# Kernel tuning notes

Hardware: AMD Instinct MI355X
Metric: run time of the kernel (lower is better)

The kernel has to match this reference:

```python
import jax, jax.numpy as jnp
import numpy as np

BN_EPS = 1e-5
DIST_EPS = 1e-8


def setup_inputs() -> dict:
    key = jax.random.key(0)
    ks = jax.random.split(key, 10)
    B, Ni, Mi = 4, 16384, 4096
    C1, C2 = 64, 64
    Cin = C1 + C2  # 128, mlp=[128,128,128]
    inp = {
        "unknown": jax.random.normal(ks[0], (B * Ni, 3), dtype=jnp.float32),
        "unknown_batch_cnt": np.full(B, Ni, dtype=np.int64),
        "known": jax.random.normal(ks[1], (B * Mi, 3), dtype=jnp.float32),
        "known_batch_cnt": np.full(B, Mi, dtype=np.int64),
        "unknown_feats": jax.random.normal(ks[2], (B * Ni, C1), dtype=jnp.float32),
        "known_feats": jax.random.normal(ks[3], (B * Mi, C2), dtype=jnp.float32),
        "W1": jax.random.normal(ks[4], (128, Cin), dtype=jnp.float32) * 0.05,
        "g1": jnp.ones((128,), dtype=jnp.float32),
        "b1": jnp.zeros((128,), dtype=jnp.float32),
        "W2": jax.random.normal(ks[5], (128, 128), dtype=jnp.float32) * 0.05,
        "g2": jnp.ones((128,), dtype=jnp.float32),
        "b2": jnp.zeros((128,), dtype=jnp.float32),
    }
    return inp


def _three_nn(u, k):
    # u: (B,Ni,3), k: (B,Mi,3) -> dist (B,Ni,3), idx (B,Ni,3) within each batch
    d2 = (jnp.sum(u * u, -1)[:, :, None] + jnp.sum(k * k, -1)[:, None, :]
          - 2.0 * jnp.einsum("bnd,bmd->bnm", u, k))  # (B,Ni,Mi)
    neg_d2, idx = jax.lax.top_k(-d2, 3)
    dist = jnp.sqrt(jnp.maximum(-neg_d2, 0.0))
    return dist, idx


def _bn_relu(y, g, b):
    # BatchNorm2d over the point dim (training-mode batch stats), then ReLU
    mu = jnp.mean(y, axis=0)
    var = jnp.mean((y - mu) ** 2, axis=0)
    return jax.nn.relu((y - mu) * jax.lax.rsqrt(var + BN_EPS) * g + b)


def reference(unknown, unknown_batch_cnt, known, known_batch_cnt,
              unknown_feats, known_feats, W1, g1, b1, W2, g2, b2):
    ucnt = np.asarray(unknown_batch_cnt)
    kcnt = np.asarray(known_batch_cnt)
    B = ucnt.shape[0]
    Ni, Mi = int(ucnt[0]), int(kcnt[0])  # equal-count ragged batches
    C2 = known_feats.shape[1]

    u = unknown.reshape(B, Ni, 3)
    k = known.reshape(B, Mi, 3)
    dist, idx = _three_nn(u, k)

    dist_recip = 1.0 / (dist + DIST_EPS)
    weight = dist_recip / jnp.sum(dist_recip, axis=-1, keepdims=True)  # (B,Ni,3)

    kf = known_feats.reshape(B, Mi, C2)
    gathered = kf[jnp.arange(B)[:, None, None], idx]  # (B,Ni,3,C2)
    interp = jnp.sum(weight[..., None] * gathered, axis=2).reshape(B * Ni, C2)

    x = jnp.concatenate([interp, unknown_feats], axis=1)  # (N, C2+C1)
    x = _bn_relu(x @ W1.T, g1, b1)
    x = _bn_relu(x @ W2.T, g2, b2)
    return x
```

## Files before the change

### kernel.cpp

```cpp
#include <hip/hip_runtime.h>
#include <hip/hip_bf16.h>

#define GRID  32
#define NCELL (GRID * GRID * GRID)
#define H     0.3125f
#define INVH  3.2f
#define OFF   5.0f
#define SUBW  8
#define XPAD  136
#define NREP  16

using f32x4  = __attribute__((ext_vector_type(4))) float;
using bf16x8 = __attribute__((ext_vector_type(8))) short;

static __device__ inline short f2bs(float f) {
  __hip_bfloat16 h = __float2bfloat16(f);
  return __builtin_bit_cast(short, h);
}
static __device__ inline float bs2f(short s) {
  return __bfloat162float(__builtin_bit_cast(__hip_bfloat16, s));
}
static __device__ inline int cellco(float x) {
  int c = (int)((x + OFF) * INVH);
  return min(GRID - 1, max(0, c));
}

#define INSF(dv, mv)                                   \
  {                                                    \
    bool q0 = dv < b0, q1 = dv < b1, q2 = dv < b2;     \
    float P0 = b0, P1 = b1; int Q0 = j0, Q1 = j1;      \
    b2 = q1 ? P1 : (q2 ? dv : b2);                     \
    j2 = q1 ? Q1 : (q2 ? mv : j2);                     \
    b1 = q0 ? P0 : (q1 ? dv : P1);                     \
    j1 = q0 ? Q0 : (q1 ? mv : Q1);                     \
    b0 = q0 ? dv : P0;                                 \
    j0 = q0 ? mv : Q0;                                 \
  }

#define MERGE3(lo_mk, hi_mk)                                                        \
  for (int mk = lo_mk; mk <= hi_mk; mk <<= 1) {                                     \
    float ob0 = __shfl_xor(b0, mk), ob1 = __shfl_xor(b1, mk), ob2 = __shfl_xor(b2, mk); \
    int   oj0 = __shfl_xor(j0, mk), oj1 = __shfl_xor(j1, mk), oj2 = __shfl_xor(j2, mk); \
    INSF(ob0, oj0); INSF(ob1, oj1); INSF(ob2, oj2);                                 \
  }

__global__ __launch_bounds__(256) void zero_k(int4* __restrict__ dst, int n4) {
  int i = blockIdx.x * 256 + threadIdx.x;
  if (i < n4) dst[i] = int4{0, 0, 0, 0};
}

__global__ __launch_bounds__(256) void hist_k(
    const float* __restrict__ known, int Mtot, int Mi,
    const float* __restrict__ unknown, int Ntot,
    int* __restrict__ khist, int* __restrict__ qhist,
    int* __restrict__ kcell, int* __restrict__ qcell,
    const float* __restrict__ W1, const float* __restrict__ W2,
    __hip_bfloat16* __restrict__ Wb1, __hip_bfloat16* __restrict__ Wb2) {
  int i = blockIdx.x * 256 + threadIdx.x;
  if (i < 128 * 128) {
    Wb1[i] = __float2bfloat16(W1[i]);
    Wb2[i] = __float2bfloat16(W2[i]);
  }
  if (i < Mtot) {
    int b = i / Mi;
    float x = known[(size_t)i * 3], y = known[(size_t)i * 3 + 1], z = known[(size_t)i * 3 + 2];
    int c = b * NCELL + (cellco(z) * GRID + cellco(y)) * GRID + cellco(x);
    kcell[i] = c;
    atomicAdd(&khist[c], 1);
  }
  if (i < Ntot) {
    int Ni = Ntot / (Mtot / Mi);
    int b = i / Ni;
    float x = unknown[(size_t)i * 3], y = unknown[(size_t)i * 3 + 1], z = unknown[(size_t)i * 3 + 2];
    int c = b * NCELL + (cellco(z) * GRID + cellco(y)) * GRID + cellco(x);
    qcell[i] = c;
    atomicAdd(&qhist[c], 1);
  }
}

__global__ __launch_bounds__(256) void scan1_k(
    const int4* __restrict__ Hc4, int* __restrict__ bsum) {
  __shared__ int sh[256];
  int t = threadIdx.x;
  int4 h = Hc4[blockIdx.x * 256 + t];
  int s = h.x + h.y + h.z + h.w;
  sh[t] = s;
  __syncthreads();
  for (int d = 128; d > 0; d >>= 1) {
    if (t < d) sh[t] += sh[t + d];
    __syncthreads();
  }
  if (t == 0) bsum[blockIdx.x] = sh[0];
}

__global__ __launch_bounds__(256) void scan2_k(
    int* __restrict__ bsum, int nb, int* __restrict__ kstart, int* __restrict__ qstart,
    int nc, int Mtot, int Ntot) {
  __shared__ int sh[256];
  int t = threadIdx.x;
  int v = (t < nb) ? bsum[t] : 0;
  sh[t] = v;
  __syncthreads();
  for (int d = 1; d < 256; d <<= 1) {
    int u = (t >= d) ? sh[t - d] : 0;
    __syncthreads();
    sh[t] += u;
    __syncthreads();
  }
  if (t < nb) bsum[t] = sh[t] - v;
  if (t == 0) { kstart[nc] = Mtot; qstart[nc] = Ntot; }
}

__global__ __launch_bounds__(256) void scan3_k(
    const int4* __restrict__ Hc4, const int* __restrict__ bsum,
    int* __restrict__ kstart, int* __restrict__ kfill,
    int* __restrict__ qstart, int* __restrict__ qfill, int nc, int Mtot) {
  __shared__ int sh[256];
  int t = threadIdx.x;
  int g4 = blockIdx.x * 256 + t;
  int4 h = Hc4[g4];
  int s = h.x + h.y + h.z + h.w;
  sh[t] = s;
  __syncthreads();
  for (int d = 1; d < 256; d <<= 1) {
    int u = (t >= d) ? sh[t - d] : 0;
    __syncthreads();
    sh[t] += u;
    __syncthreads();
  }
  int run = bsum[blockIdx.x] + sh[t] - s;
  int hv[4] = {h.x, h.y, h.z, h.w};
#pragma unroll
  for (int j = 0; j < 4; ++j) {
    int g = g4 * 4 + j;
    if (g < nc) { kstart[g] = run; kfill[g] = run; }
    else        { int q = g - nc; qstart[q] = run - Mtot; qfill[q] = run - Mtot; }
    run += hv[j];
  }
}

__global__ __launch_bounds__(256) void scatter_k(
    const float* __restrict__ known, int Mtot, int Mi,
    const float* __restrict__ unknown, int Ntot,
    const int* __restrict__ kcell, const int* __restrict__ qcell,
    int* __restrict__ kfill, int* __restrict__ qfill,
    f32x4* __restrict__ k4s, int* __restrict__ korder,
    f32x4* __restrict__ u4s, int* __restrict__ qorder) {
  int i = blockIdx.x * 256 + threadIdx.x;
  if (i < Mtot) {
    int slot = atomicAdd(&kfill[kcell[i]], 1);
    float x = known[(size_t)i * 3], y = known[(size_t)i * 3 + 1], z = known[(size_t)i * 3 + 2];
    f32x4 v;
    v[0] = -2.f * x; v[1] = -2.f * y; v[2] = -2.f * z;
    v[3] = x * x + y * y + z * z;
    k4s[slot] = v;
    korder[slot] = i - (i / Mi) * Mi;
  }
  if (i < Ntot) {
    int slot = atomicAdd(&qfill[qcell[i]], 1);
    float x = unknown[(size_t)i * 3], y = unknown[(size_t)i * 3 + 1], z = unknown[(size_t)i * 3 + 2];
    f32x4 v;
    v[0] = x; v[1] = y; v[2] = z;
    v[3] = __fmaf_rn(x, x, __fmaf_rn(y, y, z * z));
    u4s[slot] = v;
    qorder[slot] = i;
  }
}

static __device__ __forceinline__ void scan_box_strided(
    int R, int sub, int stride, int cx, int cy, int cz, int cellbase,
    const int* __restrict__ cstart, const f32x4* __restrict__ k4s,
    const int* __restrict__ korder,
    float ux, float uy, float uz,
    float& b0, float& b1, float& b2, int& j0, int& j1, int& j2) {
  int zlo = max(cz - R, 0), zhi = min(cz + R, GRID - 1);
  int ylo = max(cy - R, 0), yhi = min(cy + R, GRID - 1);
  int xlo = max(cx - R, 0), xhi = min(cx + R, GRID - 1);
  int ny = yhi - ylo + 1;
  int nrows = (zhi - zlo + 1) * ny;
  for (int rid = sub; rid < nrows; rid += stride) {
    int zz = rid / ny;
    int y  = ylo + (rid - zz * ny);
    int row = cellbase + ((zlo + zz) * GRID + y) * GRID;
    int s = cstart[row + xlo];
    int e = cstart[row + xhi + 1];
    for (int i = s; i < e; ++i) {
      f32x4 k = k4s[i];
      float d = __fmaf_rn(ux, k[0], __fmaf_rn(uy, k[1], __fmaf_rn(uz, k[2], k[3])));
      int m = korder[i];
      INSF(d, m);
    }
  }
}

__global__ __launch_bounds__(256) void knn_grid_k(
    const f32x4* __restrict__ u4s, const int* __restrict__ qorder,
    const int* __restrict__ cstart, const f32x4* __restrict__ k4s,
    const int* __restrict__ korder, int Ni,
    float* __restrict__ w, int* __restrict__ idx,
    int* __restrict__ rcnt, int* __restrict__ rlist, float* __restrict__ rd3) {
  int nwc = gridDim.x * 4;
  int gw  = blockIdx.x * 4 + (threadIdx.x >> 6);
  int wchunk = (gw * 997) & (nwc - 1);
  int s   = wchunk * 8 + ((threadIdx.x & 63) / SUBW);
  int sub = threadIdx.x & (SUBW - 1);
  f32x4 u4 = u4s[s];
  int p = qorder[s];
  int b = p / Ni;
  float ux = u4[0], uy = u4[1], uz = u4[2], uu = u4[3];
  int cx = cellco(ux), cy = cellco(uy), cz = cellco(uz);
  int cellbase = b * NCELL;
  int xlo = max(cx - 1, 0), xhi = min(cx + 1, GRID - 1);

  int cs[9], ce[9];
#pragma unroll
  for (int q = 0; q < 9; ++q) {
    int z = cz + (q / 3) - 1;
    int y = cy + (q % 3) - 1;
    bool valid = ((unsigned)z < GRID) && ((unsigned)y < GRID);
    int row = cellbase + (z * GRID + y) * GRID;
    int a0 = valid ? row + xlo : cellbase;
    int a1 = valid ? row + xhi + 1 : cellbase;
    cs[q] = cstart[a0];
    ce[q] = cstart[a1];
  }

  float b0 = 3e38f, b1 = 3e38f, b2 = 3e38f;
  int   j0 = 0,     j1 = 0,     j2 = 0;
#pragma unroll
  for (int q = 0; q < 9; ++q) {
    for (int i = cs[q] + sub; i < ce[q]; i += SUBW) {
      f32x4 k = k4s[i];
      float d = __fmaf_rn(ux, k[0], __fmaf_rn(uy, k[1], __fmaf_rn(uz, k[2], k[3])));
      int m = korder[i];
      INSF(d, m);
    }
  }
  MERGE3(1, SUBW / 2);

  float d3sq = b2 + uu;
  bool ok = d3sq <= H * H;

  if (sub == 0) {
    if (ok) {
      float d0 = sqrtf(fmaxf(b0 + uu, 0.f));
      float d1 = sqrtf(fmaxf(b1 + uu, 0.f));
      float d2 = sqrtf(fmaxf(b2 + uu, 0.f));
      float r0 = 1.f / (d0 + 1e-8f);
      float r1 = 1.f / (d1 + 1e-8f);
      float r2 = 1.f / (d2 + 1e-8f);
      float rs = 1.f / (r0 + r1 + r2);
      size_t o = (size_t)p * 3;
      w[o] = r0 * rs; w[o + 1] = r1 * rs; w[o + 2] = r2 * rs;
      idx[o] = j0; idx[o + 1] = j1; idx[o + 2] = j2;
    } else {
      int t = atomicAdd(rcnt, 1);
      rlist[t] = s;
      rd3[t] = d3sq;
    }
  }
}

__global__ __launch_bounds__(256) void knn_retry_k(
    const f32x4* __restrict__ u4s, const int* __restrict__ qorder,
    const int* __restrict__ rlist, const float* __restrict__ rd3,
    const int* __restrict__ rcnt,
    const int* __restrict__ cstart, const f32x4* __restrict__ k4s,
    const int* __restrict__ korder, int Ni,
    float* __restrict__ w, int* __restrict__ idx) {
  int lane = threadIdx.x & 63;
  int wv   = blockIdx.x * 4 + (threadIdx.x >> 6);
  int nw   = gridDim.x * 4;
  int cnt  = rcnt[0];
  for (int q = wv; q < cnt; q += nw) {
    int sq = rlist[q];
    f32x4 u4 = u4s[sq];
    int p = qorder[sq];
    int b = p / Ni;
    float ux = u4[0], uy = u4[1], uz = u4[2], uu = u4[3];
    int cx = cellco(ux), cy = cellco(uy), cz = cellco(uz);
    int cellbase = b * NCELL;

    float d3sq = rd3[q];
    int Rc = 1;
    float b0, b1, b2; int j0, j1, j2;
    bool ok = false;
    while (!ok) {
      if (d3sq < 1e30f) {
        Rc = max((int)ceilf(sqrtf(fmaxf(d3sq, 0.f)) * INVH), Rc + 1);
      } else {
        Rc = Rc * 2;
      }
      Rc = min(Rc, GRID);
      b0 = b1 = b2 = 3e38f; j0 = j1 = j2 = 0;
      scan_box_strided(Rc, lane, 64, cx, cy, cz, cellbase, cstart, k4s, korder,
                       ux, uy, uz, b0, b1, b2, j0, j1, j2);
      MERGE3(1, 32);
      d3sq = b2 + uu;
      float cov = (float)Rc * H;
      ok = (d3sq <= cov * cov) || (Rc >= GRID);
    }
    if (lane == 0) {
      float d0 = sqrtf(fmaxf(b0 + uu, 0.f));
      float d1 = sqrtf(fmaxf(b1 + uu, 0.f));
      float d2 = sqrtf(fmaxf(b2 + uu, 0.f));
      float r0 = 1.f / (d0 + 1e-8f);
      float r1 = 1.f / (d1 + 1e-8f);
      float r2 = 1.f / (d2 + 1e-8f);
      float rs = 1.f / (r0 + r1 + r2);
      size_t o = (size_t)p * 3;
      w[o] = r0 * rs; w[o + 1] = r1 * rs; w[o + 2] = r2 * rs;
      idx[o] = j0; idx[o + 1] = j1; idx[o + 2] = j2;
    }
  }
}

template <bool F32OUT>
static __device__ __forceinline__ void gemm_half(
    const short* xs, const short* Ws, int row0,
    float* yf, __hip_bfloat16* yb, float* ls, float* lq) {
  int t = threadIdx.x;
  int lane = t & 63;
  int wv = t >> 6;
  int r = lane & 15, g = lane >> 4;
  int tile = wv >> 1, half = wv & 1;
  int trow = tile * 16;

  bf16x8 a[4];
#pragma unroll
  for (int q = 0; q < 4; ++q)
    a[q] = *reinterpret_cast<const bf16x8*>(&xs[(trow + r) * XPAD + g * 8 + q * 32]);

  int orow = row0 + trow + g * 4;
#pragma unroll
  for (int ct = 0; ct < 4; ++ct) {
    int ocol = half * 64 + ct * 16 + r;
    f32x4 acc = {0.f, 0.f, 0.f, 0.f};
    size_t bbase = (size_t)ocol * 128 + g * 8;
#pragma unroll
    for (int q = 0; q < 4; ++q) {
      bf16x8 bfr = *reinterpret_cast<const bf16x8*>(Ws + bbase + q * 32);
      acc = __builtin_amdgcn_mfma_f32_16x16x32_bf16(a[q], bfr, acc, 0, 0, 0);
    }
    if (F32OUT) {
#pragma unroll
      for (int i = 0; i < 4; ++i)
        yf[(size_t)(orow + i) * 128 + ocol] = acc[i];
    } else {
#pragma unroll
      for (int i = 0; i < 4; ++i)
        yb[(size_t)(orow + i) * 128 + ocol] = __float2bfloat16(acc[i]);
    }
    float s  = acc[0] + acc[1] + acc[2] + acc[3];
    float q2 = acc[0] * acc[0] + acc[1] * acc[1] + acc[2] * acc[2] + acc[3] * acc[3];
    s  += __shfl_xor(s, 16);  s  += __shfl_xor(s, 32);
    q2 += __shfl_xor(q2, 16); q2 += __shfl_xor(q2, 32);
    if (g == 0) {
      atomicAdd(&ls[ocol], s);
      atomicAdd(&lq[ocol], q2);
    }
  }
}

__global__ __launch_bounds__(256) void gemm1_fused_k(
    const float* __restrict__ kf, const float* __restrict__ uf,
    const float* __restrict__ wgt, const int* __restrict__ idx,
    const __hip_bfloat16* __restrict__ Wb, __hip_bfloat16* __restrict__ Yb,
    float* __restrict__ stats, int Ni, int Mi) {
  __shared__ short xs[32 * XPAD];
  __shared__ float ls[128], lq[128];
  int t = threadIdx.x;
  if (t < 128) { ls[t] = 0.f; lq[t] = 0.f; }
  int row0 = blockIdx.x * 32;

  int rr = t >> 3, c0 = (t & 7) * 16;
  int p = row0 + rr;
  short tmp[16];
  if (c0 < 64) {
    size_t o = (size_t)p * 3;
    float w0 = wgt[o], w1 = wgt[o + 1], w2 = wgt[o + 2];
    int i0 = idx[o], i1 = idx[o + 1], i2 = idx[o + 2];
    int b = p / Ni;
    const float* kfb = kf + (size_t)b * Mi * 64 + c0;
    const f32x4* r0p = reinterpret_cast<const f32x4*>(kfb + (size_t)i0 * 64);
    const f32x4* r1p = reinterpret_cast<const f32x4*>(kfb + (size_t)i1 * 64);
    const f32x4* r2p = reinterpret_cast<const f32x4*>(kfb + (size_t)i2 * 64);
#pragma unroll
    for (int j = 0; j < 4; ++j) {
      f32x4 av = r0p[j], bv = r1p[j], cv = r2p[j];
#pragma unroll
      for (int e = 0; e < 4; ++e)
        tmp[j * 4 + e] = f2bs(w0 * av[e] + w1 * bv[e] + w2 * cv[e]);
    }
  } else {
    const f32x4* ufp = reinterpret_cast<const f32x4*>(uf + (size_t)p * 64 + (c0 - 64));
#pragma unroll
    for (int j = 0; j < 4; ++j) {
      f32x4 av = ufp[j];
#pragma unroll
      for (int e = 0; e < 4; ++e)
        tmp[j * 4 + e] = f2bs(av[e]);
    }
  }
  *reinterpret_cast<bf16x8*>(&xs[rr * XPAD + c0])     = *reinterpret_cast<bf16x8*>(&tmp[0]);
  *reinterpret_cast<bf16x8*>(&xs[rr * XPAD + c0 + 8]) = *reinterpret_cast<bf16x8*>(&tmp[8]);
  __syncthreads();

  gemm_half<false>(xs, reinterpret_cast<const short*>(Wb), row0, nullptr, Yb, ls, lq);

  __syncthreads();
  if (t < 128) {
    int rep = blockIdx.x & (NREP - 1);
    atomicAdd(&stats[rep * 256 + t], ls[t]);
    atomicAdd(&stats[rep * 256 + 128 + t], lq[t]);
  }
}

__global__ __launch_bounds__(256) void gemm2_bn_k(
    const __hip_bfloat16* __restrict__ Y1, const float* __restrict__ AB,
    const __hip_bfloat16* __restrict__ Wb, float* __restrict__ Yf,
    float* __restrict__ stats) {
  __shared__ short xs[32 * XPAD];
  __shared__ float ls[128], lq[128];
  int t = threadIdx.x;
  if (t < 128) { ls[t] = 0.f; lq[t] = 0.f; }
  int row0 = blockIdx.x * 32;

  int rr = t >> 3, c0 = (t & 7) * 16;
  int p = row0 + rr;
  const short* Ys = reinterpret_cast<const short*>(Y1);
  bf16x8 v0 = *reinterpret_cast<const bf16x8*>(Ys + (size_t)p * 128 + c0);
  bf16x8 v1 = *reinterpret_cast<const bf16x8*>(Ys + (size_t)p * 128 + c0 + 8);
  short tmp[16];
#pragma unroll
  for (int j = 0; j < 8; ++j)
    tmp[j] = f2bs(fmaxf(bs2f(v0[j]) * AB[c0 + j] + AB[128 + c0 + j], 0.f));
#pragma unroll
  for (int j = 0; j < 8; ++j)
    tmp[8 + j] = f2bs(fmaxf(bs2f(v1[j]) * AB[c0 + 8 + j] + AB[128 + c0 + 8 + j], 0.f));
  *reinterpret_cast<bf16x8*>(&xs[rr * XPAD + c0])     = *reinterpret_cast<bf16x8*>(&tmp[0]);
  *reinterpret_cast<bf16x8*>(&xs[rr * XPAD + c0 + 8]) = *reinterpret_cast<bf16x8*>(&tmp[8]);
  __syncthreads();

  gemm_half<true>(xs, reinterpret_cast<const short*>(Wb), row0, Yf, nullptr, ls, lq);

  __syncthreads();
  if (t < 128) {
    int rep = blockIdx.x & (NREP - 1);
    atomicAdd(&stats[rep * 256 + t], ls[t]);
    atomicAdd(&stats[rep * 256 + 128 + t], lq[t]);
  }
}

__global__ void finalize_k(const float* __restrict__ stats, const float* __restrict__ g,
                           const float* __restrict__ bb, float invN, float* __restrict__ AB) {
  int c = threadIdx.x;
  float s = 0.f, q = 0.f;
  for (int rpl = 0; rpl < NREP; ++rpl) {
    s += stats[rpl * 256 + c];
    q += stats[rpl * 256 + 128 + c];
  }
  float mu  = s * invN;
  float var = q * invN - mu * mu;
  float A = rsqrtf(var + 1e-5f) * g[c];
  AB[c] = A;
  AB[128 + c] = bb[c] - mu * A;
}

__global__ __launch_bounds__(256) void bnrelu_f32_k(
    float* __restrict__ Y, const float* __restrict__ AB, long n4) {
  long i = (long)blockIdx.x * 256 + threadIdx.x;
  long stride = (long)gridDim.x * 256;
  for (; i < n4; i += stride) {
    f32x4 y = reinterpret_cast<f32x4*>(Y)[i];
    int c0 = (int)((i * 4) & 127);
    f32x4 A  = *reinterpret_cast<const f32x4*>(AB + c0);
    f32x4 Bv = *reinterpret_cast<const f32x4*>(AB + 128 + c0);
    f32x4 o;
#pragma unroll
    for (int j = 0; j < 4; ++j) o[j] = fmaxf(y[j] * A[j] + Bv[j], 0.f);
    reinterpret_cast<f32x4*>(Y)[i] = o;
  }
}

extern "C" void kernel_launch(void* const* d_in, const int* in_sizes, int n_in,
                              void* d_out, int out_size, void* d_ws, size_t ws_size,
                              hipStream_t stream) {
  const float* unknown = (const float*)d_in[0];
  const float* known   = (const float*)d_in[2];
  const float* uf      = (const float*)d_in[4];
  const float* kf      = (const float*)d_in[5];
  const float* W1      = (const float*)d_in[6];
  const float* g1      = (const float*)d_in[7];
  const float* b1      = (const float*)d_in[8];
  const float* W2      = (const float*)d_in[9];
  const float* g2      = (const float*)d_in[10];
  const float* b2      = (const float*)d_in[11];

  int B    = in_sizes[1];
  int Ntot = in_sizes[0] / 3;
  int Mtot = in_sizes[2] / 3;
  int Ni = Ntot / B, Mi = Mtot / B;
  int nc = B * NCELL;
  int n2 = 2 * nc;

  char* ws = (char*)d_ws;
  size_t off = 0;
  auto alloc = [&](size_t bytes) {
    void* p = ws + off;
    off += (bytes + 255) & ~(size_t)255;
    return p;
  };
  float* stats  = (float*)alloc(2 * NREP * 256 * 4);
  int*   rcnt   = (int*)alloc(4);
  int*   khist  = (int*)alloc((size_t)n2 * 4);
  int*   qhist  = khist + nc;
  size_t zero_bytes = (size_t)((char*)(khist + n2) - (char*)stats);
  int*   kstart = (int*)alloc((size_t)(nc + 1) * 4);
  int*   qstart = (int*)alloc((size_t)(nc + 1) * 4);
  int*   kfill  = (int*)alloc((size_t)nc * 4);
  int*   qfill  = (int*)alloc((size_t)nc * 4);
  int*   kcell  = (int*)alloc((size_t)Mtot * 4);
  int*   qcell  = (int*)alloc((size_t)Ntot * 4);
  int*   korder = (int*)alloc((size_t)Mtot * 4);
  int*   qorder = (int*)alloc((size_t)Ntot * 4);
  int*   bsum   = (int*)alloc((size_t)(n2 / 1024) * 4);
  int*   rlist  = (int*)alloc((size_t)Ntot * 4);
  float* rd3    = (float*)alloc((size_t)Ntot * 4);
  f32x4* k4s    = (f32x4*)alloc((size_t)Mtot * 16);
  f32x4* u4s    = (f32x4*)alloc((size_t)Ntot * 16);
  float* wgt    = (float*)alloc((size_t)Ntot * 3 * 4);
  int*   idx    = (int*)alloc((size_t)Ntot * 3 * 4);
  __hip_bfloat16* y1b = (__hip_bfloat16*)alloc((size_t)Ntot * 128 * 2);
  __hip_bfloat16* Wb1 = (__hip_bfloat16*)alloc(128 * 128 * 2);
  __hip_bfloat16* Wb2 = (__hip_bfloat16*)alloc(128 * 128 * 2);
  float* AB1 = (float*)alloc(256 * 4);
  float* AB2 = (float*)alloc(256 * 4);

  float* y2 = (float*)d_out;
  long n4 = (long)Ntot * 128 / 4;
  float invN = 1.0f / (float)Ntot;
  int nb = n2 / 1024;
  float* stats2 = stats + NREP * 256;
  int zn4 = (int)(zero_bytes / 16);

  zero_k<<<(zn4 + 255) / 256, 256, 0, stream>>>((int4*)stats, zn4);
  hist_k<<<(Ntot + 255) / 256, 256, 0, stream>>>(known, Mtot, Mi, unknown, Ntot,
                                                 khist, qhist, kcell, qcell, W1, W2, Wb1, Wb2);
  scan1_k<<<nb, 256, 0, stream>>>((const int4*)khist, bsum);
  scan2_k<<<1, 256, 0, stream>>>(bsum, nb, kstart, qstart, nc, Mtot, Ntot);
  scan3_k<<<nb, 256, 0, stream>>>((const int4*)khist, bsum, kstart, kfill, qstart, qfill, nc, Mtot);
  scatter_k<<<(Ntot + 255) / 256, 256, 0, stream>>>(known, Mtot, Mi, unknown, Ntot,
                                                    kcell, qcell, kfill, qfill, k4s, korder, u4s, qorder);
  knn_grid_k<<<Ntot / 32, 256, 0, stream>>>(u4s, qorder, kstart, k4s, korder, Ni,
                                            wgt, idx, rcnt, rlist, rd3);
  knn_retry_k<<<1024, 256, 0, stream>>>(u4s, qorder, rlist, rd3, rcnt,
                                        kstart, k4s, korder, Ni, wgt, idx);
  gemm1_fused_k<<<Ntot / 32, 256, 0, stream>>>(kf, uf, wgt, idx, Wb1, y1b, stats, Ni, Mi);
  finalize_k<<<1, 128, 0, stream>>>(stats, g1, b1, invN, AB1);
  gemm2_bn_k<<<Ntot / 32, 256, 0, stream>>>(y1b, AB1, Wb2, y2, stats2);
  finalize_k<<<1, 128, 0, stream>>>(stats2, g2, b2, invN, AB2);
  bnrelu_f32_k<<<2048, 256, 0, stream>>>(y2, AB2, n4);
}
```

Before: 159.9 us.

## Stage per-batch known points in LDS for kNN and fold scan2 into scan3

The kNN grid kernel now has each block load its batch's entire known-point array (Mi float4 coords plus order indices) into shared memory and run the neighbor search from LDS instead of global memory. Blocks are remapped so each handles 32 consecutive sorted queries. Queries that fall in a different batch than the block's first query go to the retry list. The separate single-block scan2 launch is removed; every scan3 block redundantly prefix-sums the block sums itself. This saves a launch but costs about 80KB of LDS per block, which hurts occupancy, and each block reloads all 4096 points even though it touches only a few cells.

Result: no change. 160.0 us (+0.0%).

```diff
diff --git a/kernel.cpp b/kernel.cpp
--- a/kernel.cpp
+++ b/kernel.cpp
@@ -9,6 +9,7 @@
 #define SUBW  8
 #define XPAD  136
 #define NREP  16
+#define MILDS 4096
 
 using f32x4  = __attribute__((ext_vector_type(4))) float;
 using bf16x8 = __attribute__((ext_vector_type(8))) short;
@@ -93,42 +94,31 @@
   if (t == 0) bsum[blockIdx.x] = sh[0];
 }
 
-__global__ __launch_bounds__(256) void scan2_k(
-    int* __restrict__ bsum, int nb, int* __restrict__ kstart, int* __restrict__ qstart,
+__global__ __launch_bounds__(256) void scan3_k(
+    const int4* __restrict__ Hc4, const int* __restrict__ bsum, int nbk,
+    int* __restrict__ kstart, int* __restrict__ kfill,
+    int* __restrict__ qstart, int* __restrict__ qfill,
     int nc, int Mtot, int Ntot) {
   __shared__ int sh[256];
+  __shared__ int sv[256], sc[256];
   int t = threadIdx.x;
-  int v = (t < nb) ? bsum[t] : 0;
-  sh[t] = v;
-  __syncthreads();
-  for (int d = 1; d < 256; d <<= 1) {
-    int u = (t >= d) ? sh[t - d] : 0;
-    __syncthreads();
-    sh[t] += u;
-    __syncthreads();
-  }
-  if (t < nb) bsum[t] = sh[t] - v;
-  if (t == 0) { kstart[nc] = Mtot; qstart[nc] = Ntot; }
-}
-
-__global__ __launch_bounds__(256) void scan3_k(
-    const int4* __restrict__ Hc4, const int* __restrict__ bsum,
-    int* __restrict__ kstart, int* __restrict__ kfill,
-    int* __restrict__ qstart, int* __restrict__ qfill, int nc, int Mtot) {
-  __shared__ int sh[256];
-  int t = threadIdx.x;
+  int v = (t < nbk) ? bsum[t] : 0;
+  sv[t] = v; sc[t] = v;
   int g4 = blockIdx.x * 256 + t;
   int4 h = Hc4[g4];
   int s = h.x + h.y + h.z + h.w;
   sh[t] = s;
   __syncthreads();
   for (int d = 1; d < 256; d <<= 1) {
-    int u = (t >= d) ? sh[t - d] : 0;
+    int u1 = (t >= d) ? sc[t - d] : 0;
+    int u2 = (t >= d) ? sh[t - d] : 0;
     __syncthreads();
-    sh[t] += u;
+    sc[t] += u1;
+    sh[t] += u2;
     __syncthreads();
   }
-  int run = bsum[blockIdx.x] + sh[t] - s;
+  int blockbase = sc[blockIdx.x] - sv[blockIdx.x];
+  int run = blockbase + sh[t] - s;
   int hv[4] = {h.x, h.y, h.z, h.w};
 #pragma unroll
   for (int j = 0; j < 4; ++j) {
@@ -137,6 +127,7 @@
     else        { int q = g - nc; qstart[q] = run - Mtot; qfill[q] = run - Mtot; }
     run += hv[j];
   }
+  if (blockIdx.x == 0 && t == 0) { kstart[nc] = Mtot; qstart[nc] = Ntot; }
 }
 
 __global__ __launch_bounds__(256) void scatter_k(
@@ -193,23 +184,43 @@
   }
 }
 
-__global__ __launch_bounds__(256) void knn_grid_k(
+__global__ __launch_bounds__(256, 2) void knn_grid_k(
     const f32x4* __restrict__ u4s, const int* __restrict__ qorder,
     const int* __restrict__ cstart, const f32x4* __restrict__ k4s,
-    const int* __restrict__ korder, int Ni,
+    const int* __restrict__ korder, int Ni, int Mi,
     float* __restrict__ w, int* __restrict__ idx,
     int* __restrict__ rcnt, int* __restrict__ rlist, float* __restrict__ rd3) {
-  int nwc = gridDim.x * 4;
-  int gw  = blockIdx.x * 4 + (threadIdx.x >> 6);
-  int wchunk = (gw * 997) & (nwc - 1);
-  int s   = wchunk * 8 + ((threadIdx.x & 63) / SUBW);
+  __shared__ f32x4 kl[MILDS];
+  __shared__ int   ko[MILDS];
+  int nbk = gridDim.x;
+  int chunk = (blockIdx.x * 997) & (nbk - 1);
+  int s0 = chunk * 32;
+  int bb = qorder[s0] / Ni;
+  int base = bb * Mi;
+  for (int j = threadIdx.x; j < Mi; j += 256) {
+    kl[j] = k4s[base + j];
+    ko[j] = korder[base + j];
+  }
+  __syncthreads();
+
+  int s   = s0 + (threadIdx.x / SUBW);
   int sub = threadIdx.x & (SUBW - 1);
   f32x4 u4 = u4s[s];
   int p = qorder[s];
-  int b = p / Ni;
+  int pb = p / Ni;
+
+  if (pb != bb) {
+    if (sub == 0) {
+      int t = atomicAdd(rcnt, 1);
+      rlist[t] = s;
+      rd3[t] = 3e38f;
+    }
+    return;
+  }
+
   float ux = u4[0], uy = u4[1], uz = u4[2], uu = u4[3];
   int cx = cellco(ux), cy = cellco(uy), cz = cellco(uz);
-  int cellbase = b * NCELL;
+  int cellbase = pb * NCELL;
   int xlo = max(cx - 1, 0), xhi = min(cx + 1, GRID - 1);
 
   int cs[9], ce[9];
@@ -221,8 +232,8 @@
     int row = cellbase + (z * GRID + y) * GRID;
     int a0 = valid ? row + xlo : cellbase;
     int a1 = valid ? row + xhi + 1 : cellbase;
-    cs[q] = cstart[a0];
-    ce[q] = cstart[a1];
+    cs[q] = cstart[a0] - base;
+    ce[q] = cstart[a1] - base;
   }
 
   float b0 = 3e38f, b1 = 3e38f, b2 = 3e38f;
@@ -230,9 +241,9 @@
 #pragma unroll
   for (int q = 0; q < 9; ++q) {
     for (int i = cs[q] + sub; i < ce[q]; i += SUBW) {
-      f32x4 k = k4s[i];
+      f32x4 k = kl[i];
       float d = __fmaf_rn(ux, k[0], __fmaf_rn(uy, k[1], __fmaf_rn(uz, k[2], k[3])));
-      int m = korder[i];
+      int m = ko[i];
       INSF(d, m);
     }
   }
@@ -548,11 +559,11 @@
   hist_k<<<(Ntot + 255) / 256, 256, 0, stream>>>(known, Mtot, Mi, unknown, Ntot,
                                                  khist, qhist, kcell, qcell, W1, W2, Wb1, Wb2);
   scan1_k<<<nb, 256, 0, stream>>>((const int4*)khist, bsum);
-  scan2_k<<<1, 256, 0, stream>>>(bsum, nb, kstart, qstart, nc, Mtot, Ntot);
-  scan3_k<<<nb, 256, 0, stream>>>((const int4*)khist, bsum, kstart, kfill, qstart, qfill, nc, Mtot);
+  scan3_k<<<nb, 256, 0, stream>>>((const int4*)khist, bsum, nb, kstart, kfill,
+                                  qstart, qfill, nc, Mtot, Ntot);
   scatter_k<<<(Ntot + 255) / 256, 256, 0, stream>>>(known, Mtot, Mi, unknown, Ntot,
                                                     kcell, qcell, kfill, qfill, k4s, korder, u4s, qorder);
-  knn_grid_k<<<Ntot / 32, 256, 0, stream>>>(u4s, qorder, kstart, k4s, korder, Ni,
+  knn_grid_k<<<Ntot / 32, 256, 0, stream>>>(u4s, qorder, kstart, k4s, korder, Ni, Mi,
                                             wgt, idx, rcnt, rlist, rd3);
   knn_retry_k<<<1024, 256, 0, stream>>>(u4s, qorder, rlist, rd3, rcnt,
                                         kstart, k4s, korder, Ni, wgt, idx);
```
